# Performance work log

Measured on AMD Instinct MI355X. Metric: run time of the kernel, lower is better.

Reference implementation:

```python
import jax, jax.numpy as jnp
import numpy as np

N_HEADS = 16
THETA = 10000.0


def _rope_cos_sin(seq_len, head_dim):
    # freqs_cis = exp(i * pos * theta^(-2j/d)), shape (seq_len, head_dim//2)
    inv_freq = 1.0 / (THETA ** (np.arange(0, head_dim, 2, dtype=np.float32) / head_dim))
    ang = np.arange(seq_len, dtype=np.float32)[:, None] * inv_freq[None, :]
    return jnp.asarray(np.cos(ang)), jnp.asarray(np.sin(ang))


def _apply_rope(t, cos, sin):
    # t: [B, S, H, hd]; rotate consecutive pairs as complex numbers
    B, S, H, hd = t.shape
    pairs = t.reshape(B, S, H, hd // 2, 2)
    r, i = pairs[..., 0], pairs[..., 1]
    c = cos[None, :, None, :]  # [1, S, 1, hd//2]
    s = sin[None, :, None, :]
    out_r = r * c - i * s
    out_i = r * s + i * c
    return jnp.stack([out_r, out_i], axis=-1).reshape(B, S, H, hd)


def setup_inputs() -> dict:
    key = jax.random.key(0)
    ks = jax.random.split(key, 5)
    B, S, D = 2, 2048, 2048
    scale = 1.0 / np.sqrt(D)
    return {
        "x": jax.random.normal(ks[0], (B, S, D), dtype=jnp.float32),
        "wq": jax.random.normal(ks[1], (D, D), dtype=jnp.float32) * scale,
        "wk": jax.random.normal(ks[2], (D, D), dtype=jnp.float32) * scale,
        "wv": jax.random.normal(ks[3], (D, D), dtype=jnp.float32) * scale,
        "wo": jax.random.normal(ks[4], (D, D), dtype=jnp.float32) * scale,
    }


def reference(x, wq, wk, wv, wo):
    B, S, D = x.shape
    H = N_HEADS
    hd = D // H
    cos, sin = _rope_cos_sin(S, hd)

    xq = (x @ wq.T).reshape(B, S, H, hd)
    xk = (x @ wk.T).reshape(B, S, H, hd)
    xv = (x @ wv.T).reshape(B, S, H, hd)

    xq = _apply_rope(xq, cos, sin)
    xk = _apply_rope(xk, cos, sin)

    # [B, H, S, S] scores, full (non-causal) softmax as in the source
    scores = jnp.einsum("bqhd,bkhd->bhqk", xq, xk) / jnp.sqrt(jnp.float32(hd))
    attn = jax.nn.softmax(scores, axis=-1)
    out = jnp.einsum("bhqk,bkhd->bqhd", attn, xv).reshape(B, S, D)
    return out @ wo.T
```

## Files before the change

### kernel.cpp

```cpp
#include <hip/hip_runtime.h>
#include <hip/hip_bf16.h>
#include <stdint.h>


typedef __attribute__((ext_vector_type(4))) float f32x4;
typedef __attribute__((ext_vector_type(8))) short bf16x8;

typedef __attribute__((address_space(3))) unsigned int lds_u32;
typedef __attribute__((address_space(1))) const unsigned int gbl_u32;

__device__ __forceinline__ void async16(const void* g, void* l) {
  __builtin_amdgcn_global_load_lds((gbl_u32*)g, (lds_u32*)l, 16, 0, 0);
}

__device__ __forceinline__ float bf_to_f(unsigned short u) {
  union { unsigned int i; float f; } v; v.i = ((unsigned int)u) << 16; return v.f;
}
__device__ __forceinline__ unsigned short f_to_bf(float f) {
  union { float f; unsigned int i; } v; v.f = f;
  unsigned int r = v.i + 0x7FFFu + ((v.i >> 16) & 1u);
  return (unsigned short)(r >> 16);
}
__device__ __forceinline__ unsigned int cvt_pk_bf16(float lo, float hi) {
  unsigned int r;
  asm("v_cvt_pk_bf16_f32 %0, %1, %2" : "=v"(r) : "v"(lo), "v"(hi));
  return r;
}

#define B_ 2
#define S_ 2048
#define D_ 2048
#define H_ 16
#define HD_ 128

__global__ __launch_bounds__(256) void conv_all(const float* __restrict__ x,
                                                const float* __restrict__ wq,
                                                const float* __restrict__ wk,
                                                const float* __restrict__ wv,
                                                const float* __restrict__ wo,
                                                unsigned short* __restrict__ xb,
                                                unsigned short* __restrict__ wb) {
  int i = blockIdx.x * 256 + threadIdx.x;
  const float* s;
  unsigned short* d;
  int off;
  if (i < 2097152) {
    s = x; d = xb; off = i;
  } else {
    int j = i - 2097152;
    int t = j >> 20;
    off = j & 1048575;
    s = (t == 0) ? wq : (t == 1) ? wk : (t == 2) ? wv : wo;
    d = wb + (size_t)t * 4194304;
  }
  float4 v = ((const float4*)s)[off];
  uint2 o;
  o.x = (unsigned int)f_to_bf(v.x) | ((unsigned int)f_to_bf(v.y) << 16);
  o.y = (unsigned int)f_to_bf(v.z) | ((unsigned int)f_to_bf(v.w) << 16);
  ((uint2*)d)[off] = o;
}

__global__ __launch_bounds__(256) void rope_table_kernel(float* __restrict__ cosT,
                                                         float* __restrict__ sinT) {
  int i = blockIdx.x * 256 + threadIdx.x;
  int s = i >> 6, j = i & 63;
  float inv = powf(10000.0f, -(float)(2 * j) * (1.0f / 128.0f));
  float ang = (float)s * inv;
  float sv, cv;
  sincosf(ang, &sv, &cv);
  cosT[i] = cv;
  sinT[i] = sv;
}

template <int MODE>
__global__ __launch_bounds__(256, 2) void gemm_bt(const unsigned short* __restrict__ A,
                                                  const unsigned short* __restrict__ Bm,
                                                  unsigned short* __restrict__ Cb,
                                                  float* __restrict__ Cf,
                                                  const float* __restrict__ cosT,
                                                  const float* __restrict__ sinT,
                                                  int M, int N, int K) {
  __shared__ unsigned short sA[128 * 32];
  __shared__ unsigned short sB[128 * 32];
  const int tid = threadIdx.x;
  const int l = tid & 63, wv = tid >> 6;
  const int lane15 = l & 15, lhi = l >> 4;
  const int wm = wv >> 1, wn = wv & 1;
  const int bm = blockIdx.x, bn = blockIdx.y;
  const unsigned short* Ag = A + (size_t)bm * 128 * K;
  const unsigned short* Bg = Bm + (size_t)bn * 128 * K;

  f32x4 acc[4][4];
  const f32x4 zero = {0.f, 0.f, 0.f, 0.f};
#pragma unroll
  for (int i = 0; i < 4; i++)
#pragma unroll
    for (int j = 0; j < 4; j++) acc[i][j] = zero;

  for (int k0 = 0; k0 < K; k0 += 32) {
    __syncthreads();
#pragma unroll
    for (int i = 0; i < 2; i++) {
      int c = i * 256 + tid;
      int row = c >> 2, col = (c & 3) << 3;
      async16(Ag + (size_t)row * K + k0 + col, &sA[c * 8]);
      async16(Bg + (size_t)row * K + k0 + col, &sB[c * 8]);
    }
    __syncthreads();

    bf16x8 af[4], bfr[4];
#pragma unroll
    for (int i = 0; i < 4; i++)
      af[i] = *(const bf16x8*)&sA[(wm * 64 + i * 16 + lane15) * 32 + lhi * 8];
#pragma unroll
    for (int j = 0; j < 4; j++)
      bfr[j] = *(const bf16x8*)&sB[(wn * 64 + j * 16 + lane15) * 32 + lhi * 8];
#pragma unroll
    for (int i = 0; i < 4; i++)
#pragma unroll
      for (int j = 0; j < 4; j++)
        acc[i][j] = __builtin_amdgcn_mfma_f32_16x16x32_bf16(af[i], bfr[j], acc[i][j], 0, 0, 0);
  }

#pragma unroll
  for (int i = 0; i < 4; i++) {
    int m0 = bm * 128 + wm * 64 + i * 16 + lhi * 4;
#pragma unroll
    for (int j = 0; j < 4; j++) {
      int n = bn * 128 + wn * 64 + j * 16 + lane15;
      if constexpr (MODE == 0) {
#pragma unroll
        for (int r = 0; r < 4; r++) Cb[(size_t)(m0 + r) * N + n] = f_to_bf(acc[i][j][r]);
      } else if constexpr (MODE == 1) {
#pragma unroll
        for (int r = 0; r < 4; r++) Cf[(size_t)(m0 + r) * N + n] = acc[i][j][r];
      } else if constexpr (MODE == 2) {
        int s0 = m0 & (S_ - 1);
        int jp = (n & (HD_ - 1)) >> 1;
        int odd = n & 1;
#pragma unroll
        for (int r = 0; r < 4; r++) {
          float own = acc[i][j][r];
          float prt = __shfl_xor(own, 1);
          float c = cosT[(s0 + r) * 64 + jp];
          float sn = sinT[(s0 + r) * 64 + jp];
          float outv = odd ? fmaf(prt, sn, own * c) : own * c - prt * sn;
          Cb[(size_t)(m0 + r) * N + n] = f_to_bf(outv);
        }
      } else {
        int s0 = m0 & (S_ - 1);
        size_t row = (size_t)((m0 >> 11) * D_ + n);
        uint2 st;
        st.x = (unsigned int)f_to_bf(acc[i][j][0]) | ((unsigned int)f_to_bf(acc[i][j][1]) << 16);
        st.y = (unsigned int)f_to_bf(acc[i][j][2]) | ((unsigned int)f_to_bf(acc[i][j][3]) << 16);
        *(uint2*)(Cb + row * S_ + s0) = st;
      }
    }
  }
}

__global__ __launch_bounds__(512, 2) void attn_kernel(const unsigned short* __restrict__ Q,
                                                      const unsigned short* __restrict__ K,
                                                      const unsigned short* __restrict__ Vt,
                                                      unsigned short* __restrict__ ctx,
                                                      const float* __restrict__ cosT,
                                                      const float* __restrict__ sinT) {
  __shared__ unsigned short sK[2][64 * 128];
  __shared__ unsigned short sV[2][128 * 64];
  __shared__ unsigned short sP[8][32 * 72];
  const int tid = threadIdx.x, l = tid & 63, w = tid >> 6;
  const int lane15 = l & 15, lhi = l >> 4;
  const int bh = blockIdx.x * 4 + (blockIdx.y >> 3);
  const int qt = blockIdx.y & 7;
  const int b = bh >> 4, h = bh & 15;
  const int q0 = qt * 256;
  const unsigned short* Kg = K + ((size_t)(b * S_)) * D_ + h * HD_;
  const unsigned short* Vg = Vt + ((size_t)bh * HD_) * S_;
  const float scale = 0.08838834764831845f;

  const unsigned short* gp0;
  const unsigned short* gp1;
  const unsigned short* gp2;
  const unsigned short* gp3;
  unsigned int ldsOff[4];
  int gstride;
  if (w < 4) {
    const unsigned short* t0;
#pragma unroll
    for (int i = 0; i < 4; i++) {
      int row = w * 16 + i * 4 + (l >> 4);
      int colD = (l & 15) << 4;
      int colS = colD ^ ((row & 7) << 4);
      t0 = Kg + (size_t)row * D_ + (colS >> 1);
      if (i == 0) gp0 = t0; else if (i == 1) gp1 = t0; else if (i == 2) gp2 = t0; else gp3 = t0;
      ldsOff[i] = row * 256 + colD;
    }
    gstride = 64 * D_;
  } else {
    const unsigned short* t0;
#pragma unroll
    for (int i = 0; i < 4; i++) {
      int row = (w - 4) * 32 + i * 8 + (l >> 3);
      int colD = (l & 7) << 4;
      int colS = colD ^ ((row & 7) << 4);
      t0 = Vg + (size_t)row * S_ + (colS >> 1);
      if (i == 0) gp0 = t0; else if (i == 1) gp1 = t0; else if (i == 2) gp2 = t0; else gp3 = t0;
      ldsOff[i] = row * 128 + colD;
    }
    gstride = 64;
  }

  bf16x8 qf[2][4];
#pragma unroll
  for (int s = 0; s < 2; s++) {
    int s_q = q0 + w * 32 + s * 16 + lane15;
    const unsigned short* Qrow = Q + ((size_t)(b * S_ + s_q)) * D_ + h * HD_;
#pragma unroll
    for (int kc = 0; kc < 4; kc++) {
      int d0 = kc * 32 + lhi * 8;
      uint4 raw = *(const uint4*)(Qrow + d0);
      float4 cv = *(const float4*)(cosT + (size_t)s_q * 64 + (d0 >> 1));
      float4 sv = *(const float4*)(sinT + (size_t)s_q * 64 + (d0 >> 1));
      unsigned int u[4] = {raw.x, raw.y, raw.z, raw.w};
      float cc[4] = {cv.x, cv.y, cv.z, cv.w};
      float ss[4] = {sv.x, sv.y, sv.z, sv.w};
      unsigned int o[4];
#pragma unroll
      for (int p = 0; p < 4; p++) {
        float re = bf_to_f((unsigned short)(u[p] & 0xffffu));
        float im = bf_to_f((unsigned short)(u[p] >> 16));
        float orr = (re * cc[p] - im * ss[p]) * scale;
        float oi = (re * ss[p] + im * cc[p]) * scale;
        o[p] = (unsigned int)f_to_bf(orr) | ((unsigned int)f_to_bf(oi) << 16);
      }
      union { uint4 u4; bf16x8 v; } cvt;
      cvt.u4.x = o[0]; cvt.u4.y = o[1]; cvt.u4.z = o[2]; cvt.u4.w = o[3];
      qf[s][kc] = cvt.v;
    }
  }

  float mrun[2] = {-1e30f, -1e30f}, lrun[2] = {0.f, 0.f};
  const f32x4 zero = {0.f, 0.f, 0.f, 0.f};
  f32x4 oacc[2][8];
#pragma unroll
  for (int s = 0; s < 2; s++)
#pragma unroll
    for (int nf = 0; nf < 8; nf++) oacc[s][nf] = zero;

  {
    char* base = (w < 4) ? (char*)&sK[0][0] : (char*)&sV[0][0];
    async16(gp0, base + ldsOff[0]);
    async16(gp1, base + ldsOff[1]);
    async16(gp2, base + ldsOff[2]);
    async16(gp3, base + ldsOff[3]);
    gp0 += gstride; gp1 += gstride; gp2 += gstride; gp3 += gstride;
  }

  for (int t = 0; t < 32; ++t) {
    const int cur = t & 1;
    __syncthreads();
    if (t < 31) {
      char* base = (w < 4) ? (char*)&sK[cur ^ 1][0] : (char*)&sV[cur ^ 1][0];
      async16(gp0, base + ldsOff[0]);
      async16(gp1, base + ldsOff[1]);
      async16(gp2, base + ldsOff[2]);
      async16(gp3, base + ldsOff[3]);
      gp0 += gstride; gp1 += gstride; gp2 += gstride; gp3 += gstride;
    }
    const unsigned short* sKc = sK[cur];
    const unsigned short* sVc = sV[cur];

    f32x4 sacc[2][4];
#pragma unroll
    for (int s = 0; s < 2; s++)
#pragma unroll
      for (int n = 0; n < 4; n++) sacc[s][n] = zero;
    __builtin_amdgcn_s_setprio(1);
#pragma unroll
    for (int n = 0; n < 4; n++) {
      int row = n * 16 + lane15;
#pragma unroll
      for (int kc = 0; kc < 4; kc++) {
        bf16x8 kf = *(const bf16x8*)((const char*)sKc + row * 256 +
                                     ((kc * 64 + lhi * 16) ^ ((row & 7) << 4)));
        sacc[0][n] = __builtin_amdgcn_mfma_f32_16x16x32_bf16(kf, qf[0][kc], sacc[0][n], 0, 0, 0);
        sacc[1][n] = __builtin_amdgcn_mfma_f32_16x16x32_bf16(kf, qf[1][kc], sacc[1][n], 0, 0, 0);
      }
    }
    __builtin_amdgcn_s_setprio(0);

#pragma unroll
    for (int s = 0; s < 2; s++) {
      float m0 = fmaxf(fmaxf(sacc[s][0][0], sacc[s][0][1]), fmaxf(sacc[s][0][2], sacc[s][0][3]));
      float m1 = fmaxf(fmaxf(sacc[s][1][0], sacc[s][1][1]), fmaxf(sacc[s][1][2], sacc[s][1][3]));
      float m2 = fmaxf(fmaxf(sacc[s][2][0], sacc[s][2][1]), fmaxf(sacc[s][2][2], sacc[s][2][3]));
      float m3 = fmaxf(fmaxf(sacc[s][3][0], sacc[s][3][1]), fmaxf(sacc[s][3][2], sacc[s][3][3]));
      float pmax = fmaxf(fmaxf(m0, m1), fmaxf(m2, m3));
      pmax = fmaxf(pmax, __shfl_xor(pmax, 16));
      pmax = fmaxf(pmax, __shfl_xor(pmax, 32));
      if (!__all(pmax - mrun[s] <= 8.0f)) {
        float mnew = fmaxf(mrun[s], pmax);
        float alpha = __expf(mrun[s] - mnew);
        lrun[s] *= alpha;
        float af[4];
#pragma unroll
        for (int r = 0; r < 4; r++) af[r] = __shfl(alpha, lhi * 4 + r);
#pragma unroll
        for (int nf = 0; nf < 8; nf++)
#pragma unroll
          for (int r = 0; r < 4; r++) oacc[s][nf][r] *= af[r];
        mrun[s] = mnew;
      }
      const float l2e = 1.44269504f;
      float mb = mrun[s] * l2e;
      float rs = 0.f;
      float p[4][4];
#pragma unroll
      for (int n = 0; n < 4; n++)
#pragma unroll
        for (int r = 0; r < 4; r++) {
          float pv = exp2f(sacc[s][n][r] * l2e - mb);
          p[n][r] = pv;
          rs += pv;
        }
      rs += __shfl_xor(rs, 16);
      rs += __shfl_xor(rs, 32);
      lrun[s] += rs;
#pragma unroll
      for (int n = 0; n < 4; n++) {
        uint2 st;
        st.x = cvt_pk_bf16(p[n][0], p[n][1]);
        st.y = cvt_pk_bf16(p[n][2], p[n][3]);
        *(uint2*)&sP[w][(s * 16 + lane15) * 72 + n * 16 + lhi * 4] = st;
      }
    }
    asm volatile("s_waitcnt lgkmcnt(0)" ::: "memory");
    __builtin_amdgcn_sched_barrier(0);
    bf16x8 pf[2][2];
#pragma unroll
    for (int s = 0; s < 2; s++)
#pragma unroll
      for (int kc = 0; kc < 2; kc++)
        pf[s][kc] = *(const bf16x8*)&sP[w][(s * 16 + lane15) * 72 + kc * 32 + lhi * 8];

    __builtin_amdgcn_s_setprio(1);
#pragma unroll
    for (int nf = 0; nf < 8; nf++) {
      int row = nf * 16 + lane15;
#pragma unroll
      for (int kc = 0; kc < 2; kc++) {
        bf16x8 vf = *(const bf16x8*)((const char*)sVc + row * 128 +
                                     ((kc * 64 + lhi * 16) ^ ((row & 7) << 4)));
        oacc[0][nf] = __builtin_amdgcn_mfma_f32_16x16x32_bf16(pf[0][kc], vf, oacc[0][nf], 0, 0, 0);
        oacc[1][nf] = __builtin_amdgcn_mfma_f32_16x16x32_bf16(pf[1][kc], vf, oacc[1][nf], 0, 0, 0);
      }
    }
    __builtin_amdgcn_s_setprio(0);
  }

#pragma unroll
  for (int s = 0; s < 2; s++) {
    float inv = 1.0f / lrun[s];
    float invr[4];
#pragma unroll
    for (int r = 0; r < 4; r++) invr[r] = __shfl(inv, lhi * 4 + r);
    unsigned short* Og = ctx + ((size_t)(b * S_ + q0 + w * 32 + s * 16)) * D_ + h * HD_;
#pragma unroll
    for (int r = 0; r < 4; r++) {
      int qrow = lhi * 4 + r;
#pragma unroll
      for (int nf = 0; nf < 8; nf++)
        Og[(size_t)qrow * D_ + nf * 16 + lane15] = f_to_bf(oacc[s][nf][r] * invr[r]);
    }
  }
}

extern "C" void kernel_launch(void* const* d_in, const int* in_sizes, int n_in,
                              void* d_out, int out_size, void* d_ws, size_t ws_size,
                              hipStream_t stream) {
  (void)in_sizes; (void)n_in; (void)out_size; (void)ws_size;
  const float* x = (const float*)d_in[0];
  const float* wq = (const float*)d_in[1];
  const float* wk = (const float*)d_in[2];
  const float* wv = (const float*)d_in[3];
  const float* wo = (const float*)d_in[4];
  float* out = (float*)d_out;

  char* ws = (char*)d_ws;
  const size_t MB = 1024 * 1024;
  unsigned short* xb  = (unsigned short*)(ws + 0 * MB);
  unsigned short* wqb = (unsigned short*)(ws + 16 * MB);
  unsigned short* wkb = (unsigned short*)(ws + 24 * MB);
  unsigned short* wvb = (unsigned short*)(ws + 32 * MB);
  unsigned short* wob = (unsigned short*)(ws + 40 * MB);
  unsigned short* Qb  = (unsigned short*)(ws + 48 * MB);
  unsigned short* Kb  = (unsigned short*)(ws + 64 * MB);
  unsigned short* Vtb = (unsigned short*)(ws + 80 * MB);
  float* cosT = (float*)(ws + 96 * MB);
  float* sinT = (float*)(ws + 96 * MB + 524288);
  unsigned short* ctxb = xb;

  const int M = B_ * S_;

  conv_all<<<24576, 256, 0, stream>>>(x, wq, wk, wv, wo, xb, wqb);
  rope_table_kernel<<<512, 256, 0, stream>>>(cosT, sinT);

  dim3 ggrid(M / 128, D_ / 128);
  gemm_bt<0><<<ggrid, 256, 0, stream>>>(xb, wqb, Qb, nullptr, nullptr, nullptr, M, D_, D_);
  gemm_bt<2><<<ggrid, 256, 0, stream>>>(xb, wkb, Kb, nullptr, cosT, sinT, M, D_, D_);
  gemm_bt<3><<<ggrid, 256, 0, stream>>>(xb, wvb, Vtb, nullptr, nullptr, nullptr, M, D_, D_);

  attn_kernel<<<dim3(8, 32), 512, 0, stream>>>(Qb, Kb, Vtb, ctxb, cosT, sinT);

  gemm_bt<1><<<ggrid, 256, 0, stream>>>(ctxb, wob, nullptr, out, nullptr, nullptr, M, D_, D_);
}
```

Before: 318.9 us.

## Replace GEMM with 4-stage async-pipelined 128x256 tile kernel with swizzled LDS

The projection GEMMs move from a single-buffered 128x128 tile kernel, which synchronized twice per K step, to a 512-thread 128x256 tile kernel. The new kernel keeps three K-slices in flight through a 4-deep LDS ring filled by async global-to-LDS loads, with one barrier per step. It adds an XOR swizzle on LDS columns to avoid bank conflicts, raises MFMA priority with setprio, and remaps workgroups across XCDs. The aim is to hide global load latency and raise MFMA utilization. In exchange, K, N and the grid are hard-coded to 2048 and occupancy drops to one block per CU.

```diff
diff --git a/kernel.cpp b/kernel.cpp
--- a/kernel.cpp
+++ b/kernel.cpp
@@ -72,23 +72,41 @@
   sinT[i] = sv;
 }
 
+#define GK 2048
+#define GNT 64
 template <int MODE>
-__global__ __launch_bounds__(256, 2) void gemm_bt(const unsigned short* __restrict__ A,
-                                                  const unsigned short* __restrict__ Bm,
-                                                  unsigned short* __restrict__ Cb,
-                                                  float* __restrict__ Cf,
-                                                  const float* __restrict__ cosT,
-                                                  const float* __restrict__ sinT,
-                                                  int M, int N, int K) {
-  __shared__ unsigned short sA[128 * 32];
-  __shared__ unsigned short sB[128 * 32];
+__global__ __launch_bounds__(512, 1) void gemm8p(const unsigned short* __restrict__ A,
+                                                 const unsigned short* __restrict__ Bm,
+                                                 unsigned short* __restrict__ Cb,
+                                                 float* __restrict__ Cf,
+                                                 const float* __restrict__ cosT,
+                                                 const float* __restrict__ sinT) {
+  __shared__ unsigned short sA[4][128 * 32];
+  __shared__ unsigned short sB[4][256 * 32];
   const int tid = threadIdx.x;
-  const int l = tid & 63, wv = tid >> 6;
+  const int l = tid & 63, w = tid >> 6;
   const int lane15 = l & 15, lhi = l >> 4;
-  const int wm = wv >> 1, wn = wv & 1;
-  const int bm = blockIdx.x, bn = blockIdx.y;
-  const unsigned short* Ag = A + (size_t)bm * 128 * K;
-  const unsigned short* Bg = Bm + (size_t)bn * 128 * K;
+  const int wm = w >> 2, wn = w & 3;
+  const int wgn = (blockIdx.x & 7) * 32 + (blockIdx.x >> 3);
+  const int bm = wgn & 31;
+  const int bn = wgn >> 5;
+
+  const int srow = tid >> 2;
+  const int colD = (tid & 3) << 4;
+  const int colS = colD ^ (((srow >> 1) & 3) << 4);
+  const unsigned short* aSrc  = A  + ((size_t)(bm * 128 + srow)) * GK + (colS >> 1);
+  const unsigned short* bSrc0 = Bm + ((size_t)(bn * 256 + srow)) * GK + (colS >> 1);
+  const unsigned short* bSrc1 = Bm + ((size_t)(bn * 256 + 128 + srow)) * GK + (colS >> 1);
+  const unsigned int aOff  = srow * 64 + colD;
+  const unsigned int bOff0 = srow * 64 + colD;
+  const unsigned int bOff1 = (128 + srow) * 64 + colD;
+
+#define STAGE(q)                                                   \
+  do {                                                             \
+    async16(aSrc,  (char*)sA + (q) * 8192  + aOff);  aSrc  += 32;  \
+    async16(bSrc0, (char*)sB + (q) * 16384 + bOff0); bSrc0 += 32;  \
+    async16(bSrc1, (char*)sB + (q) * 16384 + bOff1); bSrc1 += 32;  \
+  } while (0)
 
   f32x4 acc[4][4];
   const f32x4 zero = {0.f, 0.f, 0.f, 0.f};
@@ -97,50 +115,71 @@
 #pragma unroll
     for (int j = 0; j < 4; j++) acc[i][j] = zero;
 
-  for (int k0 = 0; k0 < K; k0 += 32) {
-    __syncthreads();
-#pragma unroll
-    for (int i = 0; i < 2; i++) {
-      int c = i * 256 + tid;
-      int row = c >> 2, col = (c & 3) << 3;
-      async16(Ag + (size_t)row * K + k0 + col, &sA[c * 8]);
-      async16(Bg + (size_t)row * K + k0 + col, &sB[c * 8]);
-    }
-    __syncthreads();
+  const int g = (lhi * 16) ^ (((lane15 >> 1) & 3) << 4);
+  const unsigned int aRd = (wm * 64 + lane15) * 64 + g;
+  const unsigned int bRd = (wn * 64 + lane15) * 64 + g;
+
+  STAGE(0);
+  STAGE(1);
+  STAGE(2);
+  asm volatile("s_waitcnt vmcnt(6)" ::: "memory");
+  __builtin_amdgcn_s_barrier();
+  asm volatile("" ::: "memory");
+  __builtin_amdgcn_sched_barrier(0);
+
+#pragma unroll 4
+  for (int t = 0; t < GNT; ++t) {
+    if (t < GNT - 3) STAGE((t + 3) & 3);
 
     bf16x8 af[4], bfr[4];
-#pragma unroll
-    for (int i = 0; i < 4; i++)
-      af[i] = *(const bf16x8*)&sA[(wm * 64 + i * 16 + lane15) * 32 + lhi * 8];
-#pragma unroll
-    for (int j = 0; j < 4; j++)
-      bfr[j] = *(const bf16x8*)&sB[(wn * 64 + j * 16 + lane15) * 32 + lhi * 8];
-#pragma unroll
-    for (int i = 0; i < 4; i++)
-#pragma unroll
-      for (int j = 0; j < 4; j++)
-        acc[i][j] = __builtin_amdgcn_mfma_f32_16x16x32_bf16(af[i], bfr[j], acc[i][j], 0, 0, 0);
-  }
-
-#pragma unroll
-  for (int i = 0; i < 4; i++) {
-    int m0 = bm * 128 + wm * 64 + i * 16 + lhi * 4;
-#pragma unroll
-    for (int j = 0; j < 4; j++) {
-      int n = bn * 128 + wn * 64 + j * 16 + lane15;
+    const char* aBase = (const char*)sA + (t & 3) * 8192 + aRd;
+    const char* bBase = (const char*)sB + (t & 3) * 16384 + bRd;
+#pragma unroll
+    for (int mi = 0; mi < 4; mi++) af[mi] = *(const bf16x8*)(aBase + mi * 1024);
+#pragma unroll
+    for (int ni = 0; ni < 4; ni++) bfr[ni] = *(const bf16x8*)(bBase + ni * 1024);
+
+    __builtin_amdgcn_s_setprio(1);
+#pragma unroll
+    for (int mi = 0; mi < 4; mi++)
+#pragma unroll
+      for (int ni = 0; ni < 4; ni++)
+        acc[mi][ni] = __builtin_amdgcn_mfma_f32_16x16x32_bf16(af[mi], bfr[ni], acc[mi][ni], 0, 0, 0);
+    __builtin_amdgcn_s_setprio(0);
+
+    if (t <= GNT - 4) {
+      asm volatile("s_waitcnt vmcnt(6)" ::: "memory");
+    } else if (t == GNT - 3) {
+      asm volatile("s_waitcnt vmcnt(3)" ::: "memory");
+    } else {
+      asm volatile("s_waitcnt vmcnt(0)" ::: "memory");
+    }
+    __builtin_amdgcn_s_barrier();
+    asm volatile("" ::: "memory");
+    __builtin_amdgcn_sched_barrier(0);
+  }
+#undef STAGE
+
+  const int N = 2048;
+#pragma unroll
+  for (int mi = 0; mi < 4; mi++) {
+    int m0 = bm * 128 + wm * 64 + mi * 16 + lhi * 4;
+#pragma unroll
+    for (int ni = 0; ni < 4; ni++) {
+      int n = bn * 256 + wn * 64 + ni * 16 + lane15;
       if constexpr (MODE == 0) {
 #pragma unroll
-        for (int r = 0; r < 4; r++) Cb[(size_t)(m0 + r) * N + n] = f_to_bf(acc[i][j][r]);
+        for (int r = 0; r < 4; r++) Cb[(size_t)(m0 + r) * N + n] = f_to_bf(acc[mi][ni][r]);
       } else if constexpr (MODE == 1) {
 #pragma unroll
-        for (int r = 0; r < 4; r++) Cf[(size_t)(m0 + r) * N + n] = acc[i][j][r];
+        for (int r = 0; r < 4; r++) Cf[(size_t)(m0 + r) * N + n] = acc[mi][ni][r];
       } else if constexpr (MODE == 2) {
         int s0 = m0 & (S_ - 1);
         int jp = (n & (HD_ - 1)) >> 1;
         int odd = n & 1;
 #pragma unroll
         for (int r = 0; r < 4; r++) {
-          float own = acc[i][j][r];
+          float own = acc[mi][ni][r];
           float prt = __shfl_xor(own, 1);
           float c = cosT[(s0 + r) * 64 + jp];
           float sn = sinT[(s0 + r) * 64 + jp];
@@ -151,8 +190,8 @@
         int s0 = m0 & (S_ - 1);
         size_t row = (size_t)((m0 >> 11) * D_ + n);
         uint2 st;
-        st.x = (unsigned int)f_to_bf(acc[i][j][0]) | ((unsigned int)f_to_bf(acc[i][j][1]) << 16);
-        st.y = (unsigned int)f_to_bf(acc[i][j][2]) | ((unsigned int)f_to_bf(acc[i][j][3]) << 16);
+        st.x = (unsigned int)f_to_bf(acc[mi][ni][0]) | ((unsigned int)f_to_bf(acc[mi][ni][1]) << 16);
+        st.y = (unsigned int)f_to_bf(acc[mi][ni][2]) | ((unsigned int)f_to_bf(acc[mi][ni][3]) << 16);
         *(uint2*)(Cb + row * S_ + s0) = st;
       }
     }
@@ -400,17 +439,14 @@
   float* sinT = (float*)(ws + 96 * MB + 524288);
   unsigned short* ctxb = xb;
 
-  const int M = B_ * S_;
-
   conv_all<<<24576, 256, 0, stream>>>(x, wq, wk, wv, wo, xb, wqb);
   rope_table_kernel<<<512, 256, 0, stream>>>(cosT, sinT);
 
-  dim3 ggrid(M / 128, D_ / 128);
-  gemm_bt<0><<<ggrid, 256, 0, stream>>>(xb, wqb, Qb, nullptr, nullptr, nullptr, M, D_, D_);
-  gemm_bt<2><<<ggrid, 256, 0, stream>>>(xb, wkb, Kb, nullptr, cosT, sinT, M, D_, D_);
-  gemm_bt<3><<<ggrid, 256, 0, stream>>>(xb, wvb, Vtb, nullptr, nullptr, nullptr, M, D_, D_);
+  gemm8p<0><<<256, 512, 0, stream>>>(xb, wqb, Qb, nullptr, nullptr, nullptr);
+  gemm8p<2><<<256, 512, 0, stream>>>(xb, wkb, Kb, nullptr, cosT, sinT);
+  gemm8p<3><<<256, 512, 0, stream>>>(xb, wvb, Vtb, nullptr, nullptr, nullptr);
 
   attn_kernel<<<dim3(8, 32), 512, 0, stream>>>(Qb, Kb, Vtb, ctxb, cosT, sinT);
 
-  gemm_bt<1><<<ggrid, 256, 0, stream>>>(ctxb, wob, nullptr, out, nullptr, nullptr, M, D_, D_);
-}
+  gemm8p<1><<<256, 512, 0, stream>>>(ctxb, wob, nullptr, out, nullptr, nullptr);
+}
```

Result: slower. 358.4 us (+12.4%).
